# Optimization experiments

Hardware: AMD Instinct MI355X
Metric: run time of the kernel (lower is better)

The kernel has to match this reference:

```python
import jax, jax.numpy as jnp
import numpy as np

B, S, D, H = 2, 2048, 1024, 16
DK = D // H
NEG = -1e9


def setup_inputs() -> dict:
    key = jax.random.key(0)
    ks = jax.random.split(key, 11)
    s = 1.0 / np.sqrt(D)
    inp = {
        "q": jax.random.normal(ks[0], (B, S, D), jnp.float32),
        "k": jax.random.normal(ks[1], (B, S, D), jnp.float32),
        "v": jax.random.normal(ks[2], (B, S, D), jnp.float32),
        "mask": jnp.tril(jnp.ones((S, S), jnp.int32))[None, None],  # [1,1,S,S] causal
        "Wq": jax.random.normal(ks[3], (D, D), jnp.float32) * s,
        "bq": jnp.zeros((D,), jnp.float32),
        "Wk": jax.random.normal(ks[4], (D, D), jnp.float32) * s,
        "bk": jnp.zeros((D,), jnp.float32),
        "Wv": jax.random.normal(ks[5], (D, D), jnp.float32) * s,
        "bv": jnp.zeros((D,), jnp.float32),
        "Wo": jax.random.normal(ks[6], (D, D), jnp.float32) * s,
        "bo": jnp.zeros((D,), jnp.float32),
    }
    return inp


def reference(q, k, v, mask, Wq, bq, Wk, bk, Wv, bv, Wo, bo):
    # projections (torch Linear: x @ W.T + b)
    Q = q @ Wq.T + bq
    K = k @ Wk.T + bk
    V = v @ Wv.T + bv
    # [B,S,D] -> [B,H,S,DK]
    Q = Q.reshape(B, S, H, DK).transpose(0, 2, 1, 3)
    K = K.reshape(B, S, H, DK).transpose(0, 2, 1, 3)
    V = V.reshape(B, S, H, DK).transpose(0, 2, 1, 3)
    scores = jnp.einsum("bhqd,bhkd->bhqk", Q, K) / jnp.sqrt(jnp.float32(DK))
    scores = jnp.where(mask == 0, jnp.float32(NEG), scores)
    attn = jax.nn.softmax(scores, axis=-1)  # dropout p=0.0 -> identity
    x = jnp.einsum("bhqk,bhkd->bhqd", attn, V)
    x = x.transpose(0, 2, 1, 3).reshape(B, S, D)
    return x @ Wo.T + bo
```

## Files before the change

### kernel.cpp

```cpp
#include <hip/hip_runtime.h>
#include <hip/hip_bf16.h>


typedef __bf16 bf16_t;
typedef __bf16 bf16x4 __attribute__((ext_vector_type(4)));
typedef __bf16 bf16x8 __attribute__((ext_vector_type(8)));
typedef float f32x4 __attribute__((ext_vector_type(4)));

#define BB 2
#define SS 2048
#define DD 1024
#define HH 16
#define DKK 64
#define MM 4096

#define NELT ((size_t)BB * SS * DD)

__device__ __align__(16) bf16_t g_ws[4 * NELT];

#define BM 128
#define BN 128
#define BK 32
#define LDT (BK + 8)
#define LDC 136

__global__ __launch_bounds__(256) void gemm_qkv3(
    const float* __restrict__ q,  const float* __restrict__ k,  const float* __restrict__ v,
    const float* __restrict__ Wq, const float* __restrict__ Wk, const float* __restrict__ Wv,
    const float* __restrict__ bq, const float* __restrict__ bk, const float* __restrict__ bv,
    bf16_t* __restrict__ Qp, bf16_t* __restrict__ Kp, bf16_t* __restrict__ Vt)
{
    const int z = blockIdx.z;
    const float* A    = (z == 0) ? q  : (z == 1) ? k  : v;
    const float* W    = (z == 0) ? Wq : (z == 1) ? Wk : Wv;
    const float* bias = (z == 0) ? bq : (z == 1) ? bk : bv;

    __shared__ __align__(16) bf16_t smem[128 * LDC];
    bf16_t (*As)[LDT] = (bf16_t(*)[LDT])smem;
    bf16_t (*Bs)[LDT] = (bf16_t(*)[LDT])(smem + BM * LDT);
    bf16_t (*Ct)[LDC] = (bf16_t(*)[LDC])smem;

    const int tid  = threadIdx.x;
    const int wave = tid >> 6;
    const int lane = tid & 63;
    const int quad = lane >> 4;
    const int c16  = lane & 15;
    const int bm = blockIdx.x * BM;
    const int bn = blockIdx.y * BN;
    const int wm = (wave >> 1) * 64;
    const int wn = (wave & 1) * 64;

    f32x4 acc[4][4] = {};

    for (int k0 = 0; k0 < DD; k0 += BK) {
        __syncthreads();
        #pragma unroll
        for (int it = 0; it < 4; ++it) {
            int t = tid + it * 256;
            int r = t >> 3;
            int c = (t & 7) * 4;
            f32x4 a4 = *(const f32x4*)(&A[(size_t)(bm + r) * DD + k0 + c]);
            f32x4 w4 = *(const f32x4*)(&W[(size_t)(bn + r) * DD + k0 + c]);
            bf16x4 ab, wb;
            #pragma unroll
            for (int i = 0; i < 4; ++i) { ab[i] = (bf16_t)a4[i]; wb[i] = (bf16_t)w4[i]; }
            *(bf16x4*)(&As[r][c]) = ab;
            *(bf16x4*)(&Bs[r][c]) = wb;
        }
        __syncthreads();

        bf16x8 af[4], bfr[4];
        #pragma unroll
        for (int tm = 0; tm < 4; ++tm)
            af[tm] = *(const bf16x8*)(&As[wm + tm * 16 + c16][quad * 8]);
        #pragma unroll
        for (int tn = 0; tn < 4; ++tn)
            bfr[tn] = *(const bf16x8*)(&Bs[wn + tn * 16 + c16][quad * 8]);

        #pragma unroll
        for (int tm = 0; tm < 4; ++tm)
            #pragma unroll
            for (int tn = 0; tn < 4; ++tn)
                acc[tm][tn] = __builtin_amdgcn_mfma_f32_16x16x32_bf16(
                    af[tm], bfr[tn], acc[tm][tn], 0, 0, 0);
    }

    float bia[4];
    #pragma unroll
    for (int tn = 0; tn < 4; ++tn)
        bia[tn] = bias[bn + wn + tn * 16 + c16];

    if (z < 2) {
        const float osc = (z == 0) ? 0.125f : 1.0f;
        bf16_t* C = (z == 0) ? Qp : Kp;
        #pragma unroll
        for (int tm = 0; tm < 4; ++tm)
            #pragma unroll
            for (int r = 0; r < 4; ++r) {
                size_t base = (size_t)(bm + wm + tm * 16 + quad * 4 + r) * DD;
                #pragma unroll
                for (int tn = 0; tn < 4; ++tn)
                    C[base + bn + wn + tn * 16 + c16] =
                        (bf16_t)((acc[tm][tn][r] + bia[tn]) * osc);
            }
    } else {
        __syncthreads();
        #pragma unroll
        for (int tm = 0; tm < 4; ++tm)
            #pragma unroll
            for (int tn = 0; tn < 4; ++tn) {
                bf16x4 pk;
                #pragma unroll
                for (int r = 0; r < 4; ++r)
                    pk[r] = (bf16_t)(acc[tm][tn][r] + bia[tn]);
                *(bf16x4*)(&Ct[wn + tn * 16 + c16][wm + tm * 16 + quad * 4]) = pk;
            }
        __syncthreads();
        const int b_    = bm >> 11;
        const int sbase = bm & (SS - 1);
        #pragma unroll
        for (int p = 0; p < 4; ++p) {
            int col = p * 32 + (tid >> 3);
            int si  = (tid & 7) * 8;
            size_t rowoff = (size_t)(b_ * 1024 + bn + col) * SS + sbase;
            #pragma unroll
            for (int half = 0; half < 2; ++half) {
                int s = si + half * 64;
                *(bf16x8*)(&Vt[rowoff + s]) = *(const bf16x8*)(&Ct[col][s]);
            }
        }
    }
}

__global__ __launch_bounds__(256) void gemm_out(
    const bf16_t* __restrict__ A,
    const float* __restrict__ W,
    const float* __restrict__ bias,
    float* __restrict__ C)
{
    __shared__ __align__(16) bf16_t As[BM][LDT];
    __shared__ __align__(16) bf16_t Bs[BN][LDT];

    const int tid  = threadIdx.x;
    const int wave = tid >> 6;
    const int lane = tid & 63;
    const int quad = lane >> 4;
    const int c16  = lane & 15;
    const int bm = blockIdx.x * BM;
    const int bn = blockIdx.y * BN;
    const int wm = (wave >> 1) * 64;
    const int wn = (wave & 1) * 64;

    f32x4 acc[4][4] = {};

    for (int k0 = 0; k0 < DD; k0 += BK) {
        __syncthreads();
        #pragma unroll
        for (int it = 0; it < 2; ++it) {
            int t = tid + it * 256;
            int r = t >> 2;
            int c = (t & 3) * 8;
            *(bf16x8*)(&As[r][c]) =
                *(const bf16x8*)(&A[(size_t)(bm + r) * DD + k0 + c]);
        }
        #pragma unroll
        for (int it = 0; it < 4; ++it) {
            int t = tid + it * 256;
            int r = t >> 3;
            int c = (t & 7) * 4;
            f32x4 w4 = *(const f32x4*)(&W[(size_t)(bn + r) * DD + k0 + c]);
            bf16x4 wb;
            #pragma unroll
            for (int i = 0; i < 4; ++i) wb[i] = (bf16_t)w4[i];
            *(bf16x4*)(&Bs[r][c]) = wb;
        }
        __syncthreads();

        bf16x8 af[4], bfr[4];
        #pragma unroll
        for (int tm = 0; tm < 4; ++tm)
            af[tm] = *(const bf16x8*)(&As[wm + tm * 16 + c16][quad * 8]);
        #pragma unroll
        for (int tn = 0; tn < 4; ++tn)
            bfr[tn] = *(const bf16x8*)(&Bs[wn + tn * 16 + c16][quad * 8]);

        #pragma unroll
        for (int tm = 0; tm < 4; ++tm)
            #pragma unroll
            for (int tn = 0; tn < 4; ++tn)
                acc[tm][tn] = __builtin_amdgcn_mfma_f32_16x16x32_bf16(
                    af[tm], bfr[tn], acc[tm][tn], 0, 0, 0);
    }

    float bia[4];
    #pragma unroll
    for (int tn = 0; tn < 4; ++tn)
        bia[tn] = bias[bn + wn + tn * 16 + c16];

    #pragma unroll
    for (int tm = 0; tm < 4; ++tm)
        #pragma unroll
        for (int r = 0; r < 4; ++r) {
            size_t base = (size_t)(bm + wm + tm * 16 + quad * 4 + r) * DD;
            #pragma unroll
            for (int tn = 0; tn < 4; ++tn)
                C[base + bn + wn + tn * 16 + c16] = acc[tm][tn][r] + bia[tn];
        }
}

#define LDP 72

__global__ __launch_bounds__(256) void attn_fwd4(
    const bf16_t* __restrict__ Q,
    const bf16_t* __restrict__ K,
    const bf16_t* __restrict__ Vt,
    bf16_t* __restrict__ O)
{
    const int bh = blockIdx.y;
    const int b  = bh >> 4;
    const int h  = bh & 15;
    const int qbase = ((int)gridDim.x - 1 - (int)blockIdx.x) * 128;
    const int wave = threadIdx.x >> 6;
    const int lane = threadIdx.x & 63;
    const int quad = lane >> 4;
    const int c16  = lane & 15;

    __shared__ __align__(16) bf16_t Ps[4][32][LDP];

    const int qrow0w = qbase + wave * 32;
    const int kend   = qrow0w + 32;

    bf16x8 qf[2][2];
    #pragma unroll
    for (int tm = 0; tm < 2; ++tm) {
        const bf16_t* qp = Q + ((size_t)b * SS + qrow0w + tm * 16 + c16) * DD + h * DKK;
        qf[tm][0] = *(const bf16x8*)(qp + quad * 8);
        qf[tm][1] = *(const bf16x8*)(qp + 32 + quad * 8);
    }

    const bf16_t* Kb = K  + (size_t)b * SS * DD + h * DKK;
    const bf16_t* Vb = Vt + (size_t)(b * 1024 + h * DKK) * SS;

    f32x4 oacc[2][4] = {};
    float lsum[2][4] = {};

    bf16x8 kfA[4][2], kfB[4][2];
    #pragma unroll
    for (int ct = 0; ct < 4; ++ct) {
        const bf16_t* kp = Kb + (size_t)(ct * 16 + c16) * DD;
        kfA[ct][0] = *(const bf16x8*)(kp + quad * 8);
        kfA[ct][1] = *(const bf16x8*)(kp + 32 + quad * 8);
    }

    auto step = [&](int kb, bf16x8 (&kfc)[4][2], bf16x8 (&kfn)[4][2]) {
        f32x4 sc[2][4];
        #pragma unroll
        for (int tm = 0; tm < 2; ++tm)
            #pragma unroll
            for (int ct = 0; ct < 4; ++ct) {
                f32x4 s = {};
                s = __builtin_amdgcn_mfma_f32_16x16x32_bf16(qf[tm][0], kfc[ct][0], s, 0, 0, 0);
                s = __builtin_amdgcn_mfma_f32_16x16x32_bf16(qf[tm][1], kfc[ct][1], s, 0, 0, 0);
                sc[tm][ct] = s;
            }

        if (kb + 64 < kend) {
            #pragma unroll
            for (int ct = 0; ct < 4; ++ct) {
                const bf16_t* kp = Kb + (size_t)(kb + 64 + ct * 16 + c16) * DD;
                kfn[ct][0] = *(const bf16x8*)(kp + quad * 8);
                kfn[ct][1] = *(const bf16x8*)(kp + 32 + quad * 8);
            }
        }

        bf16x8 vf[4][2];
        #pragma unroll
        for (int tn = 0; tn < 4; ++tn) {
            const bf16_t* vp = Vb + (size_t)(tn * 16 + c16) * SS + kb;
            vf[tn][0] = *(const bf16x8*)(vp + quad * 8);
            vf[tn][1] = *(const bf16x8*)(vp + 32 + quad * 8);
        }

        #pragma unroll
        for (int tm = 0; tm < 2; ++tm) {
            int rbase = qrow0w + tm * 16 + quad * 4;
            #pragma unroll
            for (int ct = 0; ct < 4; ++ct) {
                int kidx = kb + ct * 16 + c16;
                #pragma unroll
                for (int r = 0; r < 4; ++r) {
                    float s = (kidx > rbase + r) ? -1e9f : sc[tm][ct][r];
                    float p = __expf(s);
                    Ps[wave][tm * 16 + quad * 4 + r][ct * 16 + c16] = (bf16_t)p;
                    lsum[tm][r] += p;
                }
            }
        }

        asm volatile("s_waitcnt lgkmcnt(0)" ::: "memory");

        #pragma unroll
        for (int tm = 0; tm < 2; ++tm) {
            bf16x8 pa0 = *(const bf16x8*)(&Ps[wave][tm * 16 + c16][quad * 8]);
            bf16x8 pa1 = *(const bf16x8*)(&Ps[wave][tm * 16 + c16][32 + quad * 8]);
            #pragma unroll
            for (int tn = 0; tn < 4; ++tn) {
                oacc[tm][tn] = __builtin_amdgcn_mfma_f32_16x16x32_bf16(pa0, vf[tn][0], oacc[tm][tn], 0, 0, 0);
                oacc[tm][tn] = __builtin_amdgcn_mfma_f32_16x16x32_bf16(pa1, vf[tn][1], oacc[tm][tn], 0, 0, 0);
            }
        }
    };

    for (int kb = 0; kb < kend; kb += 128) {
        step(kb, kfA, kfB);
        if (kb + 64 < kend) step(kb + 64, kfB, kfA);
    }

    #pragma unroll
    for (int tm = 0; tm < 2; ++tm)
        #pragma unroll
        for (int r = 0; r < 4; ++r) {
            float l = lsum[tm][r];
            #pragma unroll
            for (int off = 1; off < 16; off <<= 1)
                l += __shfl_xor(l, off, 64);
            float inv = 1.0f / l;
            int row = qrow0w + tm * 16 + quad * 4 + r;
            size_t base = ((size_t)b * SS + row) * DD + h * DKK;
            #pragma unroll
            for (int tn = 0; tn < 4; ++tn)
                O[base + tn * 16 + c16] = (bf16_t)(oacc[tm][tn][r] * inv);
        }
}

extern "C" void kernel_launch(void* const* d_in, const int* in_sizes, int n_in,
                              void* d_out, int out_size, void* d_ws, size_t ws_size,
                              hipStream_t stream) {
    (void)in_sizes; (void)n_in; (void)out_size; (void)d_ws; (void)ws_size;
    const float* q  = (const float*)d_in[0];
    const float* k  = (const float*)d_in[1];
    const float* v  = (const float*)d_in[2];
    const float* Wq = (const float*)d_in[4];
    const float* bq = (const float*)d_in[5];
    const float* Wk = (const float*)d_in[6];
    const float* bk = (const float*)d_in[7];
    const float* Wv = (const float*)d_in[8];
    const float* bv = (const float*)d_in[9];
    const float* Wo = (const float*)d_in[10];
    const float* bo = (const float*)d_in[11];

    bf16_t* ws;
    hipGetSymbolAddress((void**)&ws, HIP_SYMBOL(g_ws));
    bf16_t* Qp = ws;
    bf16_t* Kp = Qp + NELT;
    bf16_t* Vt = Kp + NELT;
    bf16_t* Xa = Vt + NELT;

    gemm_qkv3<<<dim3(MM / BM, DD / BN, 3), 256, 0, stream>>>(
        q, k, v, Wq, Wk, Wv, bq, bk, bv, Qp, Kp, Vt);

    attn_fwd4<<<dim3(SS / 128, BB * HH), 256, 0, stream>>>(Qp, Kp, Vt, Xa);

    gemm_out<<<dim3(MM / BM, DD / BN), 256, 0, stream>>>(Xa, Wo, bo, (float*)d_out);
}
```

Measured before the change: 333.7 us.

## Pre-convert inputs and weights to bf16, stage GEMM tiles via global_load_lds

Adds a separate conversion kernel that casts q, k, v and all four weight matrices to bf16 in workspace once per call. The projection and output GEMMs then load bf16 tiles directly into LDS with the async global_load_lds builtin instead of loading fp32, converting in registers and storing to LDS. This removes the repeated fp32 reads and per-tile conversion that each block redundantly performs. The cost is an extra kernel launch plus a full read/write pass over the inputs, and LDS rows lose their padding, which may introduce bank conflicts on the fragment reads.

```diff
diff --git a/kernel.cpp b/kernel.cpp
--- a/kernel.cpp
+++ b/kernel.cpp
@@ -15,29 +15,63 @@
 #define MM 4096
 
 #define NELT ((size_t)BB * SS * DD)
-
-__device__ __align__(16) bf16_t g_ws[4 * NELT];
+#define WELT ((size_t)DD * DD)
+
+__device__ __align__(16) bf16_t g_ws[7 * NELT + 4 * WELT];
+
+__device__ __forceinline__ void gld16(const bf16_t* g, bf16_t* l) {
+    __builtin_amdgcn_global_load_lds(
+        (const __attribute__((address_space(1))) void*)g,
+        (__attribute__((address_space(3))) void*)l, 16, 0, 0);
+}
+
+__global__ __launch_bounds__(256) void cvt7(
+    const float* __restrict__ q,  const float* __restrict__ k,  const float* __restrict__ v,
+    const float* __restrict__ Wq, const float* __restrict__ Wk, const float* __restrict__ Wv,
+    const float* __restrict__ Wo,
+    bf16_t* __restrict__ qb, bf16_t* __restrict__ kb, bf16_t* __restrict__ vb,
+    bf16_t* __restrict__ Wqb, bf16_t* __restrict__ Wkb, bf16_t* __restrict__ Wvb,
+    bf16_t* __restrict__ Wob)
+{
+    const float* s; bf16_t* d; size_t n;
+    switch (blockIdx.y) {
+        case 0: s = q;  d = qb;  n = NELT; break;
+        case 1: s = k;  d = kb;  n = NELT; break;
+        case 2: s = v;  d = vb;  n = NELT; break;
+        case 3: s = Wq; d = Wqb; n = WELT; break;
+        case 4: s = Wk; d = Wkb; n = WELT; break;
+        case 5: s = Wv; d = Wvb; n = WELT; break;
+        default: s = Wo; d = Wob; n = WELT; break;
+    }
+    size_t e = ((size_t)blockIdx.x * 256 + threadIdx.x) * 8;
+    if (e >= n) return;
+    f32x4 a = *(const f32x4*)(s + e);
+    f32x4 b = *(const f32x4*)(s + e + 4);
+    bf16x8 o;
+    #pragma unroll
+    for (int i = 0; i < 4; ++i) { o[i] = (bf16_t)a[i]; o[4 + i] = (bf16_t)b[i]; }
+    *(bf16x8*)(d + e) = o;
+}
 
 #define BM 128
 #define BN 128
 #define BK 32
-#define LDT (BK + 8)
 #define LDC 136
 
 __global__ __launch_bounds__(256) void gemm_qkv3(
-    const float* __restrict__ q,  const float* __restrict__ k,  const float* __restrict__ v,
-    const float* __restrict__ Wq, const float* __restrict__ Wk, const float* __restrict__ Wv,
+    const bf16_t* __restrict__ qb, const bf16_t* __restrict__ kb, const bf16_t* __restrict__ vb,
+    const bf16_t* __restrict__ Wqb, const bf16_t* __restrict__ Wkb, const bf16_t* __restrict__ Wvb,
     const float* __restrict__ bq, const float* __restrict__ bk, const float* __restrict__ bv,
     bf16_t* __restrict__ Qp, bf16_t* __restrict__ Kp, bf16_t* __restrict__ Vt)
 {
     const int z = blockIdx.z;
-    const float* A    = (z == 0) ? q  : (z == 1) ? k  : v;
-    const float* W    = (z == 0) ? Wq : (z == 1) ? Wk : Wv;
-    const float* bias = (z == 0) ? bq : (z == 1) ? bk : bv;
+    const bf16_t* A    = (z == 0) ? qb  : (z == 1) ? kb  : vb;
+    const bf16_t* W    = (z == 0) ? Wqb : (z == 1) ? Wkb : Wvb;
+    const float*  bias = (z == 0) ? bq  : (z == 1) ? bk  : bv;
 
     __shared__ __align__(16) bf16_t smem[128 * LDC];
-    bf16_t (*As)[LDT] = (bf16_t(*)[LDT])smem;
-    bf16_t (*Bs)[LDT] = (bf16_t(*)[LDT])(smem + BM * LDT);
+    bf16_t (*As)[BK] = (bf16_t(*)[BK])smem;
+    bf16_t (*Bs)[BK] = (bf16_t(*)[BK])(smem + 128 * BK);
     bf16_t (*Ct)[LDC] = (bf16_t(*)[LDC])smem;
 
     const int tid  = threadIdx.x;
@@ -50,22 +84,19 @@
     const int wm = (wave >> 1) * 64;
     const int wn = (wave & 1) * 64;
 
+    const int srow = wave * 16 + (lane >> 2);
+    const int scol = (lane & 3) * 8;
+
     f32x4 acc[4][4] = {};
 
     for (int k0 = 0; k0 < DD; k0 += BK) {
         __syncthreads();
         #pragma unroll
-        for (int it = 0; it < 4; ++it) {
-            int t = tid + it * 256;
-            int r = t >> 3;
-            int c = (t & 7) * 4;
-            f32x4 a4 = *(const f32x4*)(&A[(size_t)(bm + r) * DD + k0 + c]);
-            f32x4 w4 = *(const f32x4*)(&W[(size_t)(bn + r) * DD + k0 + c]);
-            bf16x4 ab, wb;
-            #pragma unroll
-            for (int i = 0; i < 4; ++i) { ab[i] = (bf16_t)a4[i]; wb[i] = (bf16_t)w4[i]; }
-            *(bf16x4*)(&As[r][c]) = ab;
-            *(bf16x4*)(&Bs[r][c]) = wb;
+        for (int rd = 0; rd < 2; ++rd) {
+            gld16(A + (size_t)(bm + rd * 64 + srow) * DD + k0 + scol,
+                  &As[rd * 64 + wave * 16][0]);
+            gld16(W + (size_t)(bn + rd * 64 + srow) * DD + k0 + scol,
+                  &Bs[rd * 64 + wave * 16][0]);
         }
         __syncthreads();
 
@@ -134,12 +165,12 @@
 
 __global__ __launch_bounds__(256) void gemm_out(
     const bf16_t* __restrict__ A,
-    const float* __restrict__ W,
+    const bf16_t* __restrict__ W,
     const float* __restrict__ bias,
     float* __restrict__ C)
 {
-    __shared__ __align__(16) bf16_t As[BM][LDT];
-    __shared__ __align__(16) bf16_t Bs[BN][LDT];
+    __shared__ __align__(16) bf16_t As[BM][BK];
+    __shared__ __align__(16) bf16_t Bs[BN][BK];
 
     const int tid  = threadIdx.x;
     const int wave = tid >> 6;
@@ -151,28 +182,19 @@
     const int wm = (wave >> 1) * 64;
     const int wn = (wave & 1) * 64;
 
+    const int srow = wave * 16 + (lane >> 2);
+    const int scol = (lane & 3) * 8;
+
     f32x4 acc[4][4] = {};
 
     for (int k0 = 0; k0 < DD; k0 += BK) {
         __syncthreads();
         #pragma unroll
-        for (int it = 0; it < 2; ++it) {
-            int t = tid + it * 256;
-            int r = t >> 2;
-            int c = (t & 3) * 8;
-            *(bf16x8*)(&As[r][c]) =
-                *(const bf16x8*)(&A[(size_t)(bm + r) * DD + k0 + c]);
-        }
-        #pragma unroll
-        for (int it = 0; it < 4; ++it) {
-            int t = tid + it * 256;
-            int r = t >> 3;
-            int c = (t & 7) * 4;
-            f32x4 w4 = *(const f32x4*)(&W[(size_t)(bn + r) * DD + k0 + c]);
-            bf16x4 wb;
-            #pragma unroll
-            for (int i = 0; i < 4; ++i) wb[i] = (bf16_t)w4[i];
-            *(bf16x4*)(&Bs[r][c]) = wb;
+        for (int rd = 0; rd < 2; ++rd) {
+            gld16(A + (size_t)(bm + rd * 64 + srow) * DD + k0 + scol,
+                  &As[rd * 64 + wave * 16][0]);
+            gld16(W + (size_t)(bn + rd * 64 + srow) * DD + k0 + scol,
+                  &Bs[rd * 64 + wave * 16][0]);
         }
         __syncthreads();
 
@@ -351,15 +373,25 @@
 
     bf16_t* ws;
     hipGetSymbolAddress((void**)&ws, HIP_SYMBOL(g_ws));
-    bf16_t* Qp = ws;
-    bf16_t* Kp = Qp + NELT;
-    bf16_t* Vt = Kp + NELT;
-    bf16_t* Xa = Vt + NELT;
+    bf16_t* Qp  = ws;
+    bf16_t* Kp  = Qp + NELT;
+    bf16_t* Vt  = Kp + NELT;
+    bf16_t* Xa  = Vt + NELT;
+    bf16_t* qb  = Xa + NELT;
+    bf16_t* kb  = qb + NELT;
+    bf16_t* vb  = kb + NELT;
+    bf16_t* Wqb = vb + NELT;
+    bf16_t* Wkb = Wqb + WELT;
+    bf16_t* Wvb = Wkb + WELT;
+    bf16_t* Wob = Wvb + WELT;
+
+    cvt7<<<dim3(2048, 7), 256, 0, stream>>>(q, k, v, Wq, Wk, Wv, Wo,
+                                            qb, kb, vb, Wqb, Wkb, Wvb, Wob);
 
     gemm_qkv3<<<dim3(MM / BM, DD / BN, 3), 256, 0, stream>>>(
-        q, k, v, Wq, Wk, Wv, bq, bk, bv, Qp, Kp, Vt);
+        qb, kb, vb, Wqb, Wkb, Wvb, bq, bk, bv, Qp, Kp, Vt);
 
     attn_fwd4<<<dim3(SS / 128, BB * HH), 256, 0, stream>>>(Qp, Kp, Vt, Xa);
 
-    gemm_out<<<dim3(MM / BM, DD / BN), 256, 0, stream>>>(Xa, Wo, bo, (float*)d_out);
-}
+    gemm_out<<<dim3(MM / BM, DD / BN), 256, 0, stream>>>(Xa, Wob, bo, (float*)d_out);
+}
```

Result: faster. 326.4 us (-2.2%).
